# Performance work log

Measured on AMD Instinct MI355X. Metric: run time of the kernel, lower is better.

Reference implementation:

```python
import jax, jax.numpy as jnp
import numpy as np

DIM, NH, HD = 512, 16, 32   # dim, num_heads, head_dim = dim // num_heads
WH, WW = 8, 8               # window_size
SCALE = HD ** -0.5


def _rope2(t):
    """Axial 2D rotary embedding. t: (M, WH, WW, HD). First HD/2 dims rotate
    with the height position, last HD/2 with the width position."""
    d = HD // 2
    inv_freq = 1.0 / (10000.0 ** (jnp.arange(0, d, 2, dtype=jnp.float32) / d))  # (d/2,)

    def cos_sin(n):
        ang = jnp.arange(n, dtype=jnp.float32)[:, None] * inv_freq              # (n, d/2)
        return (jnp.concatenate([jnp.cos(ang)] * 2, -1),
                jnp.concatenate([jnp.sin(ang)] * 2, -1))                        # (n, d)

    def rot_half(u):
        u1, u2 = jnp.split(u, 2, axis=-1)
        return jnp.concatenate([-u2, u1], -1)

    cos_h, sin_h = cos_sin(WH)
    cos_w, sin_w = cos_sin(WW)
    th, tw = t[..., :d], t[..., d:]
    th = th * cos_h[:, None, :] + rot_half(th) * sin_h[:, None, :]
    tw = tw * cos_w[None, :, :] + rot_half(tw) * sin_w[None, :, :]
    return jnp.concatenate([th, tw], -1)


def setup_inputs() -> dict:
    key = jax.random.key(0)
    ks = jax.random.split(key, 8)
    s = 0.02
    return {
        "x": jax.random.normal(ks[0], (8, 64, 64, DIM), dtype=jnp.float32),
        "qkv_w": jax.random.normal(ks[1], (DIM, 3 * DIM), dtype=jnp.float32) * s,
        "qkv_b": jnp.zeros((3 * DIM,), dtype=jnp.float32),
        "kv_w": jax.random.normal(ks[2], (DIM, 2 * DIM), dtype=jnp.float32) * s,
        "kv_b": jnp.zeros((2 * DIM,), dtype=jnp.float32),
        "proj_w": jax.random.normal(ks[3], (DIM, DIM), dtype=jnp.float32) * s,
        "proj_b": jnp.zeros((DIM,), dtype=jnp.float32),
    }


def reference(x, qkv_w, qkv_b, kv_w, kv_b, proj_w, proj_b):
    B, H, W, C = x.shape
    # --- hydra linear-attention branch (computed in the torch module even when
    # use_attn=True, but its result is discarded on that path) ---
    hy_k, hy_v = jnp.split(x @ kv_w + kv_b, 2, axis=-1)
    hy_k = hy_k / jnp.linalg.norm(hy_k, axis=-1, keepdims=True)
    hy_kv = (hy_k * hy_v).reshape(B, -1, C).sum(axis=-2, keepdims=True)  # (B,1,C), unused (use_attn=True)

    # --- window partition: (B,H,W,C) -> (B*nW, N, C), N = WH*WW ---
    xw = (x.reshape(B, H // WH, WH, W // WW, WW, C)
           .transpose(0, 1, 3, 2, 4, 5)
           .reshape(-1, WH * WW, C))
    B_, N, _ = xw.shape

    qkv = (xw @ qkv_w + qkv_b).reshape(B_, N, 3, NH, HD).transpose(2, 0, 3, 1, 4)
    q, k, v = qkv[0], qkv[1], qkv[2]                 # each (B_, NH, N, HD)

    q = _rope2(q.reshape(-1, WH, WW, HD)).reshape(B_, NH, N, HD)
    k = _rope2(k.reshape(-1, WH, WW, HD)).reshape(B_, NH, N, HD)

    attn = jax.nn.softmax(jnp.einsum('bhnd,bhmd->bhnm', q * SCALE, k), axis=-1)
    out = jnp.einsum('bhnm,bhmd->bhnd', attn, v)     # (B_, NH, N, HD)
    out = out.transpose(0, 2, 1, 3).reshape(B_, N, C)

    # --- window reverse: (B*nW, N, C) -> (B, H*W, C) ---
    out = (out.reshape(B, H // WH, W // WW, WH, WW, C)
              .transpose(0, 1, 3, 2, 4, 5)
              .reshape(B, H * W, C))

    out = out @ proj_w + proj_b
    return out.reshape(B, H, W, C)
```

## Files before the change

### kernel.cpp

```cpp
#include <hip/hip_runtime.h>
#include <cstdint>
#include <cstddef>

typedef float v4f  __attribute__((ext_vector_type(4)));
typedef __bf16 v8bf __attribute__((ext_vector_type(8)));
typedef __bf16 v4bf __attribute__((ext_vector_type(4)));

#define M_TOT 32768
#define KDIM  512
#define NQKV  1536
#define NPROJ 512

__device__ __constant__ float c_invf[8] = {
  1.f, 0.31622776601683794f, 0.1f, 0.031622776601683794f,
  0.01f, 0.0031622776601683794f, 0.001f, 0.00031622776601683794f };

__device__ __forceinline__ void async_copy16(const void* g, void* l) {
  __builtin_amdgcn_global_load_lds((const __attribute__((address_space(1))) void*)g,
                                   (__attribute__((address_space(3))) void*)l, 16, 0, 0);
}

__global__ __launch_bounds__(256) void transpose_cast_kernel(
    const float* __restrict__ w, __bf16* __restrict__ wt, int K, int N) {
  __shared__ __bf16 t[64 * 72];
  const int tid = threadIdx.x;
  const int n0 = blockIdx.x * 64, k0 = blockIdx.y * 64;
#pragma unroll
  for (int i = 0; i < 16; ++i) {
    int e = i * 256 + tid;
    int kk = e >> 6, nn = e & 63;
    t[nn * 72 + kk] = (__bf16)w[(size_t)(k0 + kk) * N + n0 + nn];
  }
  __syncthreads();
#pragma unroll
  for (int i = 0; i < 2; ++i) {
    int e = i * 256 + tid;
    int nn = e >> 3, kc = e & 7;
    *(v8bf*)&wt[(size_t)(n0 + nn) * K + k0 + kc * 8] = *(const v8bf*)&t[nn * 72 + kc * 8];
  }
}

#define REG_STRIDE 12288

__global__ __launch_bounds__(256, 3) void gemm_qkv_attn(
    const float* __restrict__ X,
    const __bf16* __restrict__ Bt,
    const float* __restrict__ bias,
    __bf16* __restrict__ attn_out)
{
  __shared__ __align__(16) char smem[49152];
  __bf16* As = (__bf16*)smem;
  __bf16* Bs = (__bf16*)(smem + 16384);

  const int tid  = threadIdx.x;
  const int lane = tid & 63;
  const int wave = tid >> 6;
  const int lrow = lane & 15, quad = lane >> 4;
  const int hp   = blockIdx.y & 7;
  const int mt   = (blockIdx.y & ~7) | blockIdx.x;
  const int wl   = wave >> 1, hl = wave & 1;
  const int head = hp * 2 + hl;

  int mbase[2];
#pragma unroll
  for (int l = 0; l < 2; ++l) {
    int w  = mt * 2 + l;
    int b  = w >> 6, Wr = (w >> 3) & 7, Wc = w & 7;
    mbase[l] = b * 4096 + Wr * 512 + Wc * 8;
  }

  const float4* aptrf[4]; int aoff[4];
  const __bf16* bptr[6]; __bf16* bdst[6];
#pragma unroll
  for (int i = 0; i < 4; ++i) {
    int s = i * 256 + tid;
    int row = s >> 3, c = s & 7, qc = c ^ (row & 7);
    int tok = row & 63;
    int m = mbase[row >> 6] + ((tok >> 3) << 6) + (tok & 7);
    aptrf[i] = (const float4*)(X + (size_t)m * KDIM) + qc * 2;
    aoff[i]  = (i * 256 + tid) * 8;
  }
#pragma unroll
  for (int i = 0; i < 6; ++i) {
    int s = i * 256 + tid;
    int rl = s >> 3, c = s & 7, qc = c ^ (rl & 7);
    int sel = rl >> 6, rem = rl & 63;
    int grow = sel * 512 + (hp * 2 + (rem >> 5)) * 32 + (rem & 31);
    bptr[i] = Bt + (size_t)grow * KDIM + qc * 8;
    bdst[i] = &Bs[(i * 256 + (tid & ~63)) * 8];
  }

  v4f acc[4][6] = {};

  for (int k0 = 0; k0 < KDIM; k0 += 64) {
    float4 av0[4], av1[4];
#pragma unroll
    for (int i = 0; i < 4; ++i) { av0[i] = aptrf[i][0]; av1[i] = aptrf[i][1]; aptrf[i] += 16; }
#pragma unroll
    for (int i = 0; i < 6; ++i) { async_copy16(bptr[i], bdst[i]); bptr[i] += 64; }
#pragma unroll
    for (int i = 0; i < 4; ++i) {
      v8bf r = { (__bf16)av0[i].x, (__bf16)av0[i].y, (__bf16)av0[i].z, (__bf16)av0[i].w,
                 (__bf16)av1[i].x, (__bf16)av1[i].y, (__bf16)av1[i].z, (__bf16)av1[i].w };
      *(v8bf*)&As[aoff[i]] = r;
    }
    __syncthreads();
#pragma unroll
    for (int kb = 0; kb < 2; ++kb) {
      int sx = (((kb << 2) | quad) ^ (lrow & 7)) * 8;
      v8bf af[4], bfr[6];
#pragma unroll
      for (int mi = 0; mi < 4; ++mi)
        af[mi] = *(const v8bf*)&As[(wl * 64 + mi * 16 + lrow) * 64 + sx];
#pragma unroll
      for (int j = 0; j < 6; ++j)
        bfr[j] = *(const v8bf*)&Bs[((j >> 1) * 64 + hl * 32 + (j & 1) * 16 + lrow) * 64 + sx];
#pragma unroll
      for (int mi = 0; mi < 4; ++mi)
#pragma unroll
        for (int j = 0; j < 6; ++j)
          acc[mi][j] = __builtin_amdgcn_mfma_f32_16x16x32_bf16(af[mi], bfr[j], acc[mi][j], 0, 0, 0);
    }
    __syncthreads();
  }

  __bf16* reg = (__bf16*)(smem + wave * REG_STRIDE);
  __bf16* qL = reg;
  __bf16* kL = reg + 64 * 32;
  __bf16* vL = reg + 2 * 64 * 32;

  {
    const float invf = c_invf[lrow & 7];
    float cvh[4], svh[4], cvw[4], svw[4];
#pragma unroll
    for (int mi = 0; mi < 4; ++mi)
      __sincosf((float)(mi * 2 + (quad >> 1)) * invf, &svh[mi], &cvh[mi]);
#pragma unroll
    for (int r = 0; r < 4; ++r)
      __sincosf((float)((quad & 1) * 4 + r) * invf, &svw[r], &cvw[r]);

#pragma unroll
    for (int j = 0; j < 4; ++j) {
      int sel = j >> 1, nh = j & 1;
      int hd  = nh * 16 + lrow;
      int g   = nh * 2 + (lrow >> 3);
      float bv = bias[sel * 512 + head * 32 + hd];
      __bf16* dst = sel ? kL : qL;
#pragma unroll
      for (int mi = 0; mi < 4; ++mi) {
#pragma unroll
        for (int r = 0; r < 4; ++r) {
          int tok = mi * 16 + quad * 4 + r;
          float val = acc[mi][j][r] + bv;
          float partner = __shfl_xor(val, 8);
          float cv = nh ? cvw[r] : cvh[mi];
          float sv = nh ? svw[r] : svh[mi];
          float rh = (lrow & 8) ? partner : -partner;
          val = val * cv + rh * sv;
          if (sel == 0) val *= 0.17677669529663689f;
          dst[tok * 32 + ((g ^ quad) << 3) + (lrow & 7)] = (__bf16)val;
        }
      }
    }
  }
#pragma unroll
  for (int j = 4; j < 6; ++j) {
    int hd = (j - 4) * 16 + lrow;
    float bv = bias[1024 + head * 32 + hd];
#pragma unroll
    for (int mi = 0; mi < 4; ++mi) {
      v4bf pk;
#pragma unroll
      for (int r = 0; r < 4; ++r) pk[r] = (__bf16)(acc[mi][j][r] + bv);
      int gt = mi * 2 + (quad >> 1);
      *(v4bf*)&vL[hd * 64 + ((gt ^ (lrow & 7)) << 3) + (quad & 1) * 4] = pk;
    }
  }

  const int sq = (quad ^ (lrow >> 2)) << 3;
  v8bf qf[4], kf[4];
#pragma unroll
  for (int mi = 0; mi < 4; ++mi)
    qf[mi] = *(const v8bf*)&qL[(mi * 16 + lrow) * 32 + sq];
#pragma unroll
  for (int ni = 0; ni < 4; ++ni)
    kf[ni] = *(const v8bf*)&kL[(ni * 16 + lrow) * 32 + sq];

  v4f S[4][4] = {};
#pragma unroll
  for (int ni = 0; ni < 4; ++ni)
#pragma unroll
    for (int mi = 0; mi < 4; ++mi)
      S[ni][mi] = __builtin_amdgcn_mfma_f32_16x16x32_bf16(kf[ni], qf[mi], S[ni][mi], 0, 0, 0);

#pragma unroll
  for (int mi = 0; mi < 4; ++mi) {
    float mx = S[0][mi][0];
#pragma unroll
    for (int ni = 0; ni < 4; ++ni)
#pragma unroll
      for (int r = 0; r < 4; ++r) mx = fmaxf(mx, S[ni][mi][r]);
    mx = fmaxf(mx, __shfl_xor(mx, 16));
    mx = fmaxf(mx, __shfl_xor(mx, 32));
    float sum = 0.f;
#pragma unroll
    for (int ni = 0; ni < 4; ++ni)
#pragma unroll
      for (int r = 0; r < 4; ++r) {
        float e = __expf(S[ni][mi][r] - mx);
        S[ni][mi][r] = e; sum += e;
      }
    sum += __shfl_xor(sum, 16);
    sum += __shfl_xor(sum, 32);
    float inv = 1.f / sum;
#pragma unroll
    for (int ni = 0; ni < 4; ++ni)
#pragma unroll
      for (int r = 0; r < 4; ++r) S[ni][mi][r] *= inv;
  }

  __bf16* P = reg;
#pragma unroll
  for (int mi = 0; mi < 4; ++mi) {
    int q = mi * 16 + lrow;
#pragma unroll
    for (int ni = 0; ni < 4; ++ni) {
      v4bf pk;
#pragma unroll
      for (int r = 0; r < 4; ++r) pk[r] = (__bf16)S[ni][mi][r];
      int g = ni * 2 + (quad >> 1);
      *(v4bf*)&P[q * 64 + ((g ^ (lrow & 7)) << 3) + (quad & 1) * 4] = pk;
    }
  }

  v8bf pf[4][2], vf[2][2];
#pragma unroll
  for (int mi = 0; mi < 4; ++mi)
#pragma unroll
    for (int kc = 0; kc < 2; ++kc) {
      int row = mi * 16 + lrow;
      pf[mi][kc] = *(const v8bf*)&P[row * 64 + (((kc * 4 + quad) ^ (lrow & 7)) << 3)];
    }
#pragma unroll
  for (int kc = 0; kc < 2; ++kc)
#pragma unroll
    for (int nj = 0; nj < 2; ++nj) {
      int hd = nj * 16 + lrow;
      vf[kc][nj] = *(const v8bf*)&vL[hd * 64 + (((kc * 4 + quad) ^ (lrow & 7)) << 3)];
    }

  v4f o[2][4] = {};
#pragma unroll
  for (int nj = 0; nj < 2; ++nj)
#pragma unroll
    for (int mi = 0; mi < 4; ++mi)
#pragma unroll
      for (int kc = 0; kc < 2; ++kc)
        o[nj][mi] = __builtin_amdgcn_mfma_f32_16x16x32_bf16(vf[kc][nj], pf[mi][kc], o[nj][mi], 0, 0, 0);

  const int gwin = mt * 2 + wl;
#pragma unroll
  for (int mi = 0; mi < 4; ++mi) {
    size_t rowoff = ((size_t)gwin * 64 + mi * 16 + lrow) * 512 + head * 32 + quad * 4;
#pragma unroll
    for (int nj = 0; nj < 2; ++nj) {
      v4bf pk;
#pragma unroll
      for (int r = 0; r < 4; ++r) pk[r] = (__bf16)o[nj][mi][r];
      *(v4bf*)&attn_out[rowoff + nj * 16] = pk;
    }
  }
}

__global__ __launch_bounds__(256, 4) void gemm_proj(
    const __bf16* __restrict__ A,
    const __bf16* __restrict__ Bt,
    const float* __restrict__ bias,
    float* __restrict__ out)
{
  __shared__ __align__(16) char smem[32768];
  __bf16* smemb = (__bf16*)smem;
  const int tid  = threadIdx.x;
  const int lane = tid & 63;
  const int wave = tid >> 6;
  const int lrow = lane & 15, quad = lane >> 4;

  const int lin = blockIdx.x + blockIdx.y * 4;
  const int xcd = lin & 7, idx = lin >> 3;
  const int m0  = (xcd * 32 + (idx >> 2)) * 128;
  const int n0  = (idx & 3) * 128;

  const __bf16* aptr[2]; const __bf16* bptr[2]; int adst[2], bdst[2];
#pragma unroll
  for (int i = 0; i < 2; ++i) {
    int chunk = i * 256 + tid;
    int row2 = chunk >> 3, slot = chunk & 7;
    int g = slot ^ (row2 & 7);
    int trow = row2 * 2 + (g >> 2), kgrp = g & 3;
    aptr[i] = A + (size_t)(m0 + trow) * KDIM + kgrp * 8;
    bptr[i] = Bt + (size_t)(n0 + trow) * KDIM + kgrp * 8;
    adst[i] = (i * 256 + (tid & ~63)) * 8;
    bdst[i] = 4096 + adst[i];
  }

#pragma unroll
  for (int i = 0; i < 2; ++i) {
    async_copy16(aptr[i], smemb + adst[i]);
    async_copy16(bptr[i], smemb + bdst[i]);
  }

  v4f acc[8][2] = {};
  const int slot8 = ((((lrow & 1) << 2) | quad) ^ (lrow >> 1)) << 3;
  const int lr2 = lrow >> 1;

#pragma unroll
  for (int t = 0; t < 16; ++t) {
    __syncthreads();
    if (t < 15) {
      int nb  = ((t + 1) & 1) * 8192;
      int kof = (t + 1) * 32;
#pragma unroll
      for (int i = 0; i < 2; ++i) {
        async_copy16(aptr[i] + kof, smemb + nb + adst[i]);
        async_copy16(bptr[i] + kof, smemb + nb + bdst[i]);
      }
    }
    const __bf16* Ac = smemb + (t & 1) * 8192;
    const __bf16* Bc = Ac + 4096;
    v8bf af[2], bfr[8];
#pragma unroll
    for (int mi = 0; mi < 2; ++mi)
      af[mi] = *(const v8bf*)&Ac[(wave * 16 + mi * 8 + lr2) * 64 + slot8];
#pragma unroll
    for (int ni = 0; ni < 8; ++ni)
      bfr[ni] = *(const v8bf*)&Bc[(ni * 8 + lr2) * 64 + slot8];
    __builtin_amdgcn_s_setprio(1);
#pragma unroll
    for (int ni = 0; ni < 8; ++ni)
#pragma unroll
      for (int mi = 0; mi < 2; ++mi)
        acc[ni][mi] = __builtin_amdgcn_mfma_f32_16x16x32_bf16(bfr[ni], af[mi], acc[ni][mi], 0, 0, 0);
    __builtin_amdgcn_s_setprio(0);
  }

  float4 bv[8];
#pragma unroll
  for (int ni = 0; ni < 8; ++ni)
    bv[ni] = *(const float4*)&bias[n0 + ni * 16 + quad * 4];

  const int mb = m0 + wave * 32;
#pragma unroll
  for (int mi = 0; mi < 2; ++mi) {
    int m    = mb + mi * 16 + lrow;
    int win  = m >> 6, tok = m & 63;
    int bb   = win >> 6;
    int hblk = (win >> 3) & 7, wblk = win & 7;
    int h    = hblk * 8 + (tok >> 3);
    int w    = wblk * 8 + (tok & 7);
    float* orow = &out[(((size_t)bb * 64 + h) * 64 + w) * 512 + n0 + quad * 4];
#pragma unroll
    for (int ni = 0; ni < 8; ++ni) {
      float4 v = { acc[ni][mi][0] + bv[ni].x, acc[ni][mi][1] + bv[ni].y,
                   acc[ni][mi][2] + bv[ni].z, acc[ni][mi][3] + bv[ni].w };
      *(float4*)&orow[ni * 16] = v;
    }
  }
}

extern "C" void kernel_launch(void* const* d_in, const int* in_sizes, int n_in,
                              void* d_out, int out_size, void* d_ws, size_t ws_size,
                              hipStream_t stream) {
  (void)in_sizes; (void)n_in; (void)out_size; (void)ws_size;
  const float* x      = (const float*)d_in[0];
  const float* qkv_w  = (const float*)d_in[1];
  const float* qkv_b  = (const float*)d_in[2];
  const float* proj_w = (const float*)d_in[5];
  const float* proj_b = (const float*)d_in[6];
  float* out = (float*)d_out;

  char* ws = (char*)d_ws;
  size_t off = 0;
  auto alloc = [&](size_t bytes) {
    char* p = ws + off;
    off += (bytes + 255) & ~(size_t)255;
    return (void*)p;
  };
  __bf16* qkv_wt   = (__bf16*)alloc((size_t)NQKV * KDIM * 2);
  __bf16* proj_wt  = (__bf16*)alloc((size_t)KDIM * KDIM * 2);
  __bf16* attn_out = (__bf16*)alloc((size_t)M_TOT * KDIM * 2);

  transpose_cast_kernel<<<dim3(NQKV / 64, KDIM / 64), dim3(256), 0, stream>>>(
      qkv_w, qkv_wt, KDIM, NQKV);
  transpose_cast_kernel<<<dim3(NPROJ / 64, KDIM / 64), dim3(256), 0, stream>>>(
      proj_w, proj_wt, KDIM, NPROJ);

  gemm_qkv_attn<<<dim3(8, 256), dim3(256), 0, stream>>>(
      x, qkv_wt, qkv_b, attn_out);

  gemm_proj<<<dim3(4, 256), dim3(256), 0, stream>>>(
      attn_out, proj_wt, proj_b, out);
}
```

Measured before the change: 223.5 us.

## Pre-cast X to bf16 in fused prep kernel and async-load A tiles

Adds a prep kernel that converts the full fp32 input X to a bf16 buffer and also does both weight transpose-casts, replacing two launches with one. The QKV GEMM then loads A tiles straight into LDS with global_load_lds, the same way it already loads B, instead of loading fp32 into registers, converting, and storing to LDS. The aim is to cut per-block register and VALU pressure and read half the bytes in the GEMM. The cost is an extra full pass over X: a 64MB read and a 32MB bf16 write plus reread.

```diff
diff --git a/kernel.cpp b/kernel.cpp
--- a/kernel.cpp
+++ b/kernel.cpp
@@ -20,11 +20,34 @@
                                    (__attribute__((address_space(3))) void*)l, 16, 0, 0);
 }
 
-__global__ __launch_bounds__(256) void transpose_cast_kernel(
-    const float* __restrict__ w, __bf16* __restrict__ wt, int K, int N) {
+__global__ __launch_bounds__(256) void prep_kernel(
+    const float* __restrict__ x,      __bf16* __restrict__ xb,
+    const float* __restrict__ qkv_w,  __bf16* __restrict__ qkv_wt,
+    const float* __restrict__ proj_w, __bf16* __restrict__ proj_wt) {
+  const int tid = threadIdx.x;
+  const int bx  = blockIdx.x;
+  if (bx < 2048) {
+    const int n8 = M_TOT * KDIM / 8;
+    for (int i = bx * 256 + tid; i < n8; i += 2048 * 256) {
+      const float4* p = (const float4*)x + (size_t)i * 2;
+      float4 a = p[0], b = p[1];
+      v8bf r = { (__bf16)a.x, (__bf16)a.y, (__bf16)a.z, (__bf16)a.w,
+                 (__bf16)b.x, (__bf16)b.y, (__bf16)b.z, (__bf16)b.w };
+      *(v8bf*)(xb + (size_t)i * 8) = r;
+    }
+    return;
+  }
+  const float* w; __bf16* wt; int N, n0, k0;
+  if (bx < 2048 + 192) {
+    int idx = bx - 2048;
+    w = qkv_w; wt = qkv_wt; N = NQKV;
+    n0 = (idx % 24) * 64; k0 = (idx / 24) * 64;
+  } else {
+    int idx = bx - 2048 - 192;
+    w = proj_w; wt = proj_wt; N = NPROJ;
+    n0 = (idx % 8) * 64; k0 = (idx / 8) * 64;
+  }
   __shared__ __bf16 t[64 * 72];
-  const int tid = threadIdx.x;
-  const int n0 = blockIdx.x * 64, k0 = blockIdx.y * 64;
 #pragma unroll
   for (int i = 0; i < 16; ++i) {
     int e = i * 256 + tid;
@@ -36,14 +59,14 @@
   for (int i = 0; i < 2; ++i) {
     int e = i * 256 + tid;
     int nn = e >> 3, kc = e & 7;
-    *(v8bf*)&wt[(size_t)(n0 + nn) * K + k0 + kc * 8] = *(const v8bf*)&t[nn * 72 + kc * 8];
+    *(v8bf*)&wt[(size_t)(n0 + nn) * KDIM + k0 + kc * 8] = *(const v8bf*)&t[nn * 72 + kc * 8];
   }
 }
 
 #define REG_STRIDE 12288
 
 __global__ __launch_bounds__(256, 3) void gemm_qkv_attn(
-    const float* __restrict__ X,
+    const __bf16* __restrict__ A,
     const __bf16* __restrict__ Bt,
     const float* __restrict__ bias,
     __bf16* __restrict__ attn_out)
@@ -69,7 +92,7 @@
     mbase[l] = b * 4096 + Wr * 512 + Wc * 8;
   }
 
-  const float4* aptrf[4]; int aoff[4];
+  const __bf16* aptr[4]; __bf16* adst[4];
   const __bf16* bptr[6]; __bf16* bdst[6];
 #pragma unroll
   for (int i = 0; i < 4; ++i) {
@@ -77,8 +100,8 @@
     int row = s >> 3, c = s & 7, qc = c ^ (row & 7);
     int tok = row & 63;
     int m = mbase[row >> 6] + ((tok >> 3) << 6) + (tok & 7);
-    aptrf[i] = (const float4*)(X + (size_t)m * KDIM) + qc * 2;
-    aoff[i]  = (i * 256 + tid) * 8;
+    aptr[i] = A + (size_t)m * KDIM + qc * 8;
+    adst[i] = &As[(i * 256 + (tid & ~63)) * 8];
   }
 #pragma unroll
   for (int i = 0; i < 6; ++i) {
@@ -93,17 +116,10 @@
   v4f acc[4][6] = {};
 
   for (int k0 = 0; k0 < KDIM; k0 += 64) {
-    float4 av0[4], av1[4];
-#pragma unroll
-    for (int i = 0; i < 4; ++i) { av0[i] = aptrf[i][0]; av1[i] = aptrf[i][1]; aptrf[i] += 16; }
+#pragma unroll
+    for (int i = 0; i < 4; ++i) { async_copy16(aptr[i], adst[i]); aptr[i] += 64; }
 #pragma unroll
     for (int i = 0; i < 6; ++i) { async_copy16(bptr[i], bdst[i]); bptr[i] += 64; }
-#pragma unroll
-    for (int i = 0; i < 4; ++i) {
-      v8bf r = { (__bf16)av0[i].x, (__bf16)av0[i].y, (__bf16)av0[i].z, (__bf16)av0[i].w,
-                 (__bf16)av1[i].x, (__bf16)av1[i].y, (__bf16)av1[i].z, (__bf16)av1[i].w };
-      *(v8bf*)&As[aoff[i]] = r;
-    }
     __syncthreads();
 #pragma unroll
     for (int kb = 0; kb < 2; ++kb) {
@@ -385,17 +401,16 @@
     off += (bytes + 255) & ~(size_t)255;
     return (void*)p;
   };
+  __bf16* xb       = (__bf16*)alloc((size_t)M_TOT * KDIM * 2);
   __bf16* qkv_wt   = (__bf16*)alloc((size_t)NQKV * KDIM * 2);
   __bf16* proj_wt  = (__bf16*)alloc((size_t)KDIM * KDIM * 2);
   __bf16* attn_out = (__bf16*)alloc((size_t)M_TOT * KDIM * 2);
 
-  transpose_cast_kernel<<<dim3(NQKV / 64, KDIM / 64), dim3(256), 0, stream>>>(
-      qkv_w, qkv_wt, KDIM, NQKV);
-  transpose_cast_kernel<<<dim3(NPROJ / 64, KDIM / 64), dim3(256), 0, stream>>>(
-      proj_w, proj_wt, KDIM, NPROJ);
+  prep_kernel<<<dim3(2048 + 192 + 64), dim3(256), 0, stream>>>(
+      x, xb, qkv_w, qkv_wt, proj_w, proj_wt);
 
   gemm_qkv_attn<<<dim3(8, 256), dim3(256), 0, stream>>>(
-      x, qkv_wt, qkv_b, attn_out);
+      xb, qkv_wt, qkv_b, attn_out);
 
   gemm_proj<<<dim3(4, 256), dim3(256), 0, stream>>>(
       attn_out, proj_wt, proj_b, out);
```

After: 220.3 us. No clear change (-1.4%).
